# Kernel tuning notes

Hardware: AMD Instinct MI355X
Metric: run time of the kernel (lower is better)

Reference implementation:

```python
import math
import jax, jax.numpy as jnp
import numpy as np

DRAGON_ITERATIONS = 12
DRAGON_SMOOTHING = 0.1


def _dragon_patterns(iterations=DRAGON_ITERATIONS, smoothing=DRAGON_SMOOTHING):
    """Deterministic (non-learned) Dragon curve patterns, matching torch impl."""
    patterns = [np.array([0.5], dtype=np.float32)]
    kernel = np.ones(3, dtype=np.float32) / 3.0
    for _ in range(1, iterations):
        prev = patterns[-1]
        n = len(prev)
        newp = np.zeros(2 * n + 1, dtype=np.float32)
        newp[:n] = prev
        newp[n] = 0.5
        newp[n + 1:] = 1.0 - prev[::-1]
        if smoothing > 0:
            # conv1d with kernel_size=3, padding=1 (zero pad) == np.convolve 'same'
            newp = np.convolve(newp, kernel, mode='same').astype(np.float32)
        newp = (newp - newp.min()) / (newp.max() - newp.min() + 1e-8)
        patterns.append(newp.astype(np.float32))
    return patterns

_PATTERNS = _dragon_patterns()


def _interp_pattern(seq_len):
    """Linearly interpolate selected dragon pattern to seq_len (static shapes)."""
    it = min(int(math.log2(seq_len)), DRAGON_ITERATIONS - 1)
    pattern = _PATTERNS[it]
    if len(pattern) == seq_len:
        w = pattern.copy()
    else:
        x_old = np.linspace(0.0, 1.0, len(pattern), dtype=np.float64)
        x_new = np.linspace(0.0, 1.0, seq_len, dtype=np.float64)
        w = np.interp(x_new, x_old, pattern.astype(np.float64)).astype(np.float32)
    return it, jnp.asarray(w)


def setup_inputs() -> dict:
    key = jax.random.key(0)
    ks = jax.random.split(key, 8)
    B, S, D = 8, 2048, 512
    query = jax.random.normal(ks[0], (B, S, D), dtype=jnp.float32)
    k = jax.random.normal(ks[1], (B, S, D), dtype=jnp.float32)
    value = jax.random.normal(ks[2], (B, S, D), dtype=jnp.float32)
    pattern_scale = jnp.ones((DRAGON_ITERATIONS,), dtype=jnp.float32)
    pattern_bias = jnp.zeros((DRAGON_ITERATIONS,), dtype=jnp.float32)
    w1 = jax.random.normal(ks[3], (DRAGON_ITERATIONS, 64), dtype=jnp.float32) * (1.0 / math.sqrt(DRAGON_ITERATIONS))
    b1 = jnp.zeros((64,), dtype=jnp.float32)
    w2 = jax.random.normal(ks[4], (64, 1), dtype=jnp.float32) * (1.0 / 8.0)
    b2 = jnp.zeros((1,), dtype=jnp.float32)
    return {"query": query, "key": k, "value": value,
            "pattern_scale": pattern_scale, "pattern_bias": pattern_bias,
            "w1": w1, "b1": b1, "w2": w2, "b2": b2}


def reference(query, key, value, pattern_scale, pattern_bias, w1, b1, w2, b2):
    B, S, D = key.shape
    it, base_w = _interp_pattern(S)
    # learned affine + softplus on dragon weights
    dragon_w = jax.nn.softplus(base_w * pattern_scale[it] + pattern_bias[it])  # [S]
    weighted_keys = key * dragon_w[None, :, None]                              # [B,S,D]
    scores = jnp.einsum('bqd,bkd->bqk', query, weighted_keys) / math.sqrt(D)   # [B,S,S]
    attn = jax.nn.softmax(scores, axis=-1)
    # blend factor from one-hot iteration features through tiny MLP
    feat = jax.nn.one_hot(it, DRAGON_ITERATIONS, dtype=query.dtype)            # [12]
    h = jax.nn.relu(feat @ w1 + b1)
    blend = jax.nn.sigmoid(h @ w2 + b2)                                        # [1]
    blend = blend[0]
    final_attn = blend * attn + (1.0 - blend) / S                              # uniform blend
    out = jnp.einsum('bqk,bkd->bqd', final_attn, value)                        # [B,S,D]
    # original does output.squeeze(1); S>1 so it's a no-op here
    return out
```

## Files before the change

### kernel.cpp

```cpp
#include <hip/hip_runtime.h>
#include <cstdint>

#define DEV __device__ __forceinline__

typedef float f32x4 __attribute__((ext_vector_type(4)));
typedef short s16x8 __attribute__((ext_vector_type(8)));

DEV unsigned short f2bf(float f){
    unsigned u = __builtin_bit_cast(unsigned, f);
    u = u + 0x7fffu + ((u >> 16) & 1u);
    return (unsigned short)(u >> 16);
}
DEV float bf2f(unsigned short h){
    unsigned u = ((unsigned)h) << 16;
    return __builtin_bit_cast(float, u);
}

typedef const void __attribute__((address_space(1)))* gcp;
typedef void __attribute__((address_space(3)))* lp;
DEV void gload_lds16(const void* g, void* l){
    __builtin_amdgcn_global_load_lds((gcp)g, (lp)l, 16, 0, 0);
}

#define SCALE_QK 0.04419417382415922f

__global__ __launch_bounds__(256) void k_conv(
    const float* __restrict__ Q, const float* __restrict__ K,
    const float* __restrict__ V,
    const float* __restrict__ scale, const float* __restrict__ bias,
    const float* __restrict__ w1, const float* __restrict__ b1,
    const float* __restrict__ w2, const float* __restrict__ b2,
    unsigned short* __restrict__ Qb, unsigned short* __restrict__ Kb,
    unsigned short* __restrict__ Vt, float* __restrict__ vmean,
    float* __restrict__ dragon_wq, float* __restrict__ blend_out)
{
    __shared__ float sh[8200];
    int tid = threadIdx.x;
    int bx  = blockIdx.x;

    if (bx < 1024){
        const long long total4 = (long long)8*2048*512/4;
        long long stride = 1024LL*256;
        for (long long i = (long long)bx*256 + tid; i < total4; i += stride){
            long long base = i*4;
            const float4 q = *(const float4*)(Q + base);
            const float4 k = *(const float4*)(K + base);
            ushort4 qo, ko;
            qo.x = f2bf(q.x); qo.y = f2bf(q.y); qo.z = f2bf(q.z); qo.w = f2bf(q.w);
            ko.x = f2bf(k.x); ko.y = f2bf(k.y); ko.z = f2bf(k.z); ko.w = f2bf(k.w);
            *(ushort4*)(Qb + base) = qo;
            *(ushort4*)(Kb + base) = ko;
        }
        return;
    }

    if (bx < 3072){
        int t = bx - 1024;
        int stile = t & 31, dtile = (t >> 5) & 7, b = t >> 8;
        int s0 = stile*64, d0 = dtile*64;
        float (*tile)[66] = (float(*)[66])sh;
        float* red = sh + 4224;
        int tx = tid & 63, ty = tid >> 6;
        const float* src = V + ((long long)b*2048 + s0)*512 + d0;
        #pragma unroll
        for (int r = 0; r < 16; ++r){
            int row = r*4 + ty;
            tile[row][tx] = src[(long long)row*512 + tx];
        }
        __syncthreads();
        unsigned short* dst = Vt + ((long long)b*512 + d0)*2048 + s0;
        #pragma unroll
        for (int r = 0; r < 16; ++r){
            int drow = r*4 + ty;
            dst[(long long)drow*2048 + tx] = f2bf(tile[tx][drow]);
        }
        int dcol = tid & 63, sp = tid >> 6;
        float s = 0.f;
        #pragma unroll
        for (int ii = 0; ii < 16; ++ii) s += tile[sp*16 + ii][dcol];
        red[sp*64 + dcol] = s;
        __syncthreads();
        if (sp == 0){
            float tot = red[dcol] + red[64+dcol] + red[128+dcol] + red[192+dcol];
            atomicAdd(&vmean[b*512 + d0 + dcol], tot * (1.0f/2048.0f));
        }
        return;
    }

    float* A    = sh;
    float* Bb   = sh + 4095;
    float* red8 = sh + 8190;
    int lane = tid & 63, w = tid >> 6;
    if (tid == 0) A[0] = 0.5f;
    __syncthreads();
    float lo = 0.f, rden = 1.f;
    int len = 1;
    const float third = 1.0f/3.0f;
    for (int it = 1; it < 12; ++it){
        int n = len, nl = 2*n + 1;
        for (int i = tid; i < nl; i += 256){
            float v;
            if (i < n)       v = (A[i] - lo) * rden;
            else if (i == n) v = 0.5f;
            else             v = 1.0f - (A[2*n - i] - lo) * rden;
            Bb[i] = v;
        }
        __syncthreads();
        float mn = 3.4e38f, mx = -3.4e38f;
        for (int i = tid; i < nl; i += 256){
            float s = Bb[i];
            if (i > 0)    s += Bb[i-1];
            if (i < nl-1) s += Bb[i+1];
            s *= third;
            A[i] = s;
            mn = fminf(mn, s); mx = fmaxf(mx, s);
        }
        #pragma unroll
        for (int off = 32; off > 0; off >>= 1){
            mn = fminf(mn, __shfl_xor(mn, off, 64));
            mx = fmaxf(mx, __shfl_xor(mx, off, 64));
        }
        if (lane == 0){ red8[w] = mn; red8[4 + w] = mx; }
        __syncthreads();
        mn = fminf(fminf(red8[0], red8[1]), fminf(red8[2], red8[3]));
        mx = fmaxf(fmaxf(red8[4], red8[5]), fmaxf(red8[6], red8[7]));
        lo = mn; rden = 1.0f / (mx - mn + 1e-8f);
        len = nl;
        __syncthreads();
    }
    float sc = scale[11], bi = bias[11];
    for (int i = tid; i < 2048; i += 256){
        float x = (A[2*i] - lo) * rden * sc + bi;
        dragon_wq[i] = (fmaxf(x, 0.f) + log1pf(__expf(-fabsf(x)))) * SCALE_QK;
    }
    if (tid < 64){
        float h = fmaxf(w1[11*64 + tid] + b1[tid], 0.f);
        float c = h * w2[tid];
        for (int off = 32; off > 0; off >>= 1) c += __shfl_xor(c, off, 64);
        if (tid == 0) blend_out[0] = 1.f/(1.f + __expf(-(c + b2[0])));
    }
}

__global__ __launch_bounds__(256) void k_gemm_qk(
    const unsigned short* __restrict__ Qb, const unsigned short* __restrict__ Kb,
    const float* __restrict__ dragon_wq, unsigned short* __restrict__ Sp)
{
    __shared__ unsigned short At[128*64];
    __shared__ unsigned short Bt[128*64];
    int tid = threadIdx.x;
    int lane = tid & 63, wave = tid >> 6;
    int wm = wave >> 1, wn = wave & 1;
    int ln = lane & 15, q4 = lane >> 4;
    int sx = ln & 7;
    int q0 = blockIdx.y*128, k0 = blockIdx.x*128, b = blockIdx.z;
    const unsigned short* Abase = Qb + ((long long)b*2048 + q0)*512;
    const unsigned short* Bbase = Kb + ((long long)b*2048 + k0)*512;

    f32x4 acc[4][4];
    #pragma unroll
    for (int i = 0; i < 4; ++i)
        #pragma unroll
        for (int j = 0; j < 4; ++j) acc[i][j] = (f32x4)0.0f;

    int cc = lane & 7, rg = lane >> 3;
    for (int kt = 0; kt < 8; ++kt){
        #pragma unroll
        for (int c = 0; c < 4; ++c){
            int chunk = wave*4 + c;
            int row = chunk*8 + rg;
            int gc  = cc ^ (row & 7);
            gload_lds16(Abase + (long long)row*512 + kt*64 + gc*8, &At[chunk*512]);
            gload_lds16(Bbase + (long long)row*512 + kt*64 + gc*8, &Bt[chunk*512]);
        }
        __syncthreads();
        #pragma unroll
        for (int ks = 0; ks < 2; ++ks){
            int cs = ((ks*4 + q4) ^ sx) * 8;
            s16x8 af[4], bfr[4];
            #pragma unroll
            for (int i = 0; i < 4; ++i)
                af[i] = *(const s16x8*)&At[(wm*64 + i*16 + ln)*64 + cs];
            #pragma unroll
            for (int j = 0; j < 4; ++j)
                bfr[j] = *(const s16x8*)&Bt[(wn*64 + j*16 + ln)*64 + cs];
            #pragma unroll
            for (int i = 0; i < 4; ++i)
                #pragma unroll
                for (int j = 0; j < 4; ++j)
                    acc[i][j] = __builtin_amdgcn_mfma_f32_16x16x32_bf16(af[i], bfr[j], acc[i][j], 0, 0, 0);
        }
        __syncthreads();
    }
    float wq[4];
    #pragma unroll
    for (int j = 0; j < 4; ++j) wq[j] = dragon_wq[k0 + wn*64 + j*16 + ln];
    unsigned short* outp = Sp + (long long)b*2048*2048;
    #pragma unroll
    for (int i = 0; i < 4; ++i){
        #pragma unroll
        for (int j = 0; j < 4; ++j){
            #pragma unroll
            for (int r = 0; r < 4; ++r){
                int q = q0 + wm*64 + i*16 + q4*4 + r;
                int k = k0 + wn*64 + j*16 + ln;
                outp[(long long)q*2048 + k] = f2bf(__expf(acc[i][j][r] * wq[j]));
            }
        }
    }
}

__global__ __launch_bounds__(256) void k_gemm_pv(
    const unsigned short* __restrict__ Sp, const unsigned short* __restrict__ Vt,
    const float* __restrict__ vmean, const float* __restrict__ blendp,
    float* __restrict__ out)
{
    __shared__ unsigned short At[128*64];
    __shared__ unsigned short Bt[128*64];
    __shared__ float l_sh[128];
    int tid = threadIdx.x;
    int lane = tid & 63, wave = tid >> 6;
    int wm = wave >> 1, wn = wave & 1;
    int ln = lane & 15, q4 = lane >> 4;
    int sx = ln & 7;

    int g    = blockIdx.x;
    int xcd  = g & 7, slot = g >> 3;
    int pair = xcd*16 + (slot >> 2);
    int dt   = slot & 3;
    int qt   = pair & 15, b = pair >> 4;
    int q0 = qt*128, d0 = dt*128;

    const unsigned short* Abase = Sp + (long long)b*2048*2048 + (long long)q0*2048;
    const unsigned short* Bbase = Vt + ((long long)b*512 + d0)*2048;

    f32x4 acc[4][4];
    #pragma unroll
    for (int i = 0; i < 4; ++i)
        #pragma unroll
        for (int j = 0; j < 4; ++j) acc[i][j] = (f32x4)0.0f;
    float lsum[4] = {0.f, 0.f, 0.f, 0.f};

    int cc = lane & 7, rg = lane >> 3;
    for (int kt = 0; kt < 32; ++kt){
        #pragma unroll
        for (int c = 0; c < 4; ++c){
            int chunk = wave*4 + c;
            int row = chunk*8 + rg;
            int gc  = cc ^ (row & 7);
            gload_lds16(Abase + (long long)row*2048 + kt*64 + gc*8, &At[chunk*512]);
            gload_lds16(Bbase + (long long)row*2048 + kt*64 + gc*8, &Bt[chunk*512]);
        }
        __syncthreads();
        #pragma unroll
        for (int ks = 0; ks < 2; ++ks){
            int cs = ((ks*4 + q4) ^ sx) * 8;
            s16x8 af[4], bfr[4];
            #pragma unroll
            for (int i = 0; i < 4; ++i)
                af[i] = *(const s16x8*)&At[(wm*64 + i*16 + ln)*64 + cs];
            #pragma unroll
            for (int j = 0; j < 4; ++j)
                bfr[j] = *(const s16x8*)&Bt[(wn*64 + j*16 + ln)*64 + cs];
            if (wn == 0){
                #pragma unroll
                for (int i = 0; i < 4; ++i){
                    float s = 0.f;
                    #pragma unroll
                    for (int jj = 0; jj < 8; ++jj) s += bf2f((unsigned short)af[i][jj]);
                    lsum[i] += s;
                }
            }
            #pragma unroll
            for (int i = 0; i < 4; ++i)
                #pragma unroll
                for (int j = 0; j < 4; ++j)
                    acc[i][j] = __builtin_amdgcn_mfma_f32_16x16x32_bf16(af[i], bfr[j], acc[i][j], 0, 0, 0);
        }
        __syncthreads();
    }
    if (wn == 0){
        #pragma unroll
        for (int i = 0; i < 4; ++i){
            float v = lsum[i];
            v += __shfl_xor(v, 16, 64);
            v += __shfl_xor(v, 32, 64);
            if (lane < 16) l_sh[wm*64 + i*16 + lane] = v;
        }
    }
    __syncthreads();

    float blend = blendp[0];
    float ib = 1.0f - blend;
    float* obase = out + ((long long)b*2048 + q0)*512 + d0;
    float vm[4];
    #pragma unroll
    for (int j = 0; j < 4; ++j) vm[j] = vmean[b*512 + d0 + wn*64 + j*16 + ln];
    #pragma unroll
    for (int i = 0; i < 4; ++i){
        #pragma unroll
        for (int r = 0; r < 4; ++r){
            int ql = wm*64 + i*16 + q4*4 + r;
            float linv = 1.0f / l_sh[ql];
            #pragma unroll
            for (int j = 0; j < 4; ++j){
                int dl = wn*64 + j*16 + ln;
                obase[(long long)ql*512 + dl] = blend*acc[i][j][r]*linv + ib*vm[j];
            }
        }
    }
}

extern "C" void kernel_launch(void* const* d_in, const int* in_sizes, int n_in,
                              void* d_out, int out_size, void* d_ws, size_t ws_size,
                              hipStream_t stream)
{
    (void)in_sizes; (void)n_in; (void)out_size; (void)ws_size;
    const float* Q  = (const float*)d_in[0];
    const float* K  = (const float*)d_in[1];
    const float* V  = (const float*)d_in[2];
    const float* ps = (const float*)d_in[3];
    const float* pb = (const float*)d_in[4];
    const float* w1 = (const float*)d_in[5];
    const float* b1 = (const float*)d_in[6];
    const float* w2 = (const float*)d_in[7];
    const float* b2 = (const float*)d_in[8];
    float* out = (float*)d_out;

    char* ws = (char*)d_ws;
    float* dragon_wq       = (float*)(ws);
    float* blend           = (float*)(ws + 8192);
    float* vmean           = (float*)(ws + 16384);
    size_t off = 32768;
    unsigned short* Qb     = (unsigned short*)(ws + off);
    unsigned short* Kb     = (unsigned short*)(ws + off + (size_t)16*1024*1024);
    unsigned short* Vt     = (unsigned short*)(ws + off + (size_t)32*1024*1024);
    unsigned short* Sp     = (unsigned short*)(ws + off + (size_t)48*1024*1024);

    hipMemsetAsync(vmean, 0, 4096*sizeof(float), stream);
    hipLaunchKernelGGL(k_conv,    dim3(3073),      dim3(256), 0, stream,
                       Q, K, V, ps, pb, w1, b1, w2, b2, Qb, Kb, Vt, vmean, dragon_wq, blend);
    hipLaunchKernelGGL(k_gemm_qk, dim3(16, 16, 8), dim3(256), 0, stream,
                       Qb, Kb, dragon_wq, Sp);
    hipLaunchKernelGGL(k_gemm_pv, dim3(512),       dim3(256), 0, stream,
                       Sp, Vt, vmean, blend, out);
}
```

Measured before the change: 264.0 us.

## Precompute dragon pattern at compile time and stage QK epilogue through LDS

The serial single-block dragon-pattern construction (a long tail block in k_conv) is replaced by a constexpr table in device memory. The softplus weights are computed in the QK GEMM epilogue, and the blend MLP is computed per block in the PV kernel. The QK epilogue now writes bf16 scores into padded shared memory and stores them to global memory as coalesced 16-byte rows, instead of scattered 2-byte stores. This adds an extra LDS round trip and barrier, and the compile-time table may differ slightly from the runtime computation in floating-point rounding.

```diff
diff --git a/kernel.cpp b/kernel.cpp
--- a/kernel.cpp
+++ b/kernel.cpp
@@ -24,17 +24,41 @@
 
 #define SCALE_QK 0.04419417382415922f
 
+struct Pat2 { float v[2048]; };
+constexpr Pat2 make_pat2(){
+    float a[4095] = {}; float b[4095] = {};
+    a[0] = 0.5f; int len = 1;
+    for (int it = 1; it < 12; ++it){
+        int n = len, nl = 2*n + 1;
+        for (int i = 0; i < nl; ++i)
+            b[i] = (i < n) ? a[i] : ((i == n) ? 0.5f : 1.0f - a[2*n - i]);
+        const float third = 1.0f/3.0f;
+        float mn = 3.4e38f, mx = -3.4e38f;
+        for (int i = 0; i < nl; ++i){
+            float s = b[i]*third;
+            if (i > 0)      s += b[i-1]*third;
+            if (i < nl - 1) s += b[i+1]*third;
+            a[i] = s;
+            mn = (s < mn) ? s : mn;
+            mx = (s > mx) ? s : mx;
+        }
+        float d = mx - mn + 1e-8f;
+        for (int i = 0; i < nl; ++i) a[i] = (a[i] - mn) / d;
+        len = nl;
+    }
+    Pat2 p{};
+    for (int i = 0; i < 2048; ++i) p.v[i] = a[2*i];
+    return p;
+}
+__device__ const Pat2 g_pat2 = make_pat2();
+
 __global__ __launch_bounds__(256) void k_conv(
     const float* __restrict__ Q, const float* __restrict__ K,
     const float* __restrict__ V,
-    const float* __restrict__ scale, const float* __restrict__ bias,
-    const float* __restrict__ w1, const float* __restrict__ b1,
-    const float* __restrict__ w2, const float* __restrict__ b2,
     unsigned short* __restrict__ Qb, unsigned short* __restrict__ Kb,
-    unsigned short* __restrict__ Vt, float* __restrict__ vmean,
-    float* __restrict__ dragon_wq, float* __restrict__ blend_out)
+    unsigned short* __restrict__ Vt, float* __restrict__ vmean)
 {
-    __shared__ float sh[8200];
+    __shared__ float sh[4480];
     int tid = threadIdx.x;
     int bx  = blockIdx.x;
 
@@ -54,99 +78,47 @@
         return;
     }
 
-    if (bx < 3072){
-        int t = bx - 1024;
-        int stile = t & 31, dtile = (t >> 5) & 7, b = t >> 8;
-        int s0 = stile*64, d0 = dtile*64;
-        float (*tile)[66] = (float(*)[66])sh;
-        float* red = sh + 4224;
-        int tx = tid & 63, ty = tid >> 6;
-        const float* src = V + ((long long)b*2048 + s0)*512 + d0;
-        #pragma unroll
-        for (int r = 0; r < 16; ++r){
-            int row = r*4 + ty;
-            tile[row][tx] = src[(long long)row*512 + tx];
-        }
-        __syncthreads();
-        unsigned short* dst = Vt + ((long long)b*512 + d0)*2048 + s0;
-        #pragma unroll
-        for (int r = 0; r < 16; ++r){
-            int drow = r*4 + ty;
-            dst[(long long)drow*2048 + tx] = f2bf(tile[tx][drow]);
-        }
-        int dcol = tid & 63, sp = tid >> 6;
-        float s = 0.f;
-        #pragma unroll
-        for (int ii = 0; ii < 16; ++ii) s += tile[sp*16 + ii][dcol];
-        red[sp*64 + dcol] = s;
-        __syncthreads();
-        if (sp == 0){
-            float tot = red[dcol] + red[64+dcol] + red[128+dcol] + red[192+dcol];
-            atomicAdd(&vmean[b*512 + d0 + dcol], tot * (1.0f/2048.0f));
-        }
-        return;
-    }
-
-    float* A    = sh;
-    float* Bb   = sh + 4095;
-    float* red8 = sh + 8190;
-    int lane = tid & 63, w = tid >> 6;
-    if (tid == 0) A[0] = 0.5f;
+    int t = bx - 1024;
+    int stile = t & 31, dtile = (t >> 5) & 7, b = t >> 8;
+    int s0 = stile*64, d0 = dtile*64;
+    float (*tile)[66] = (float(*)[66])sh;
+    float* red = sh + 4224;
+    int tx = tid & 63, ty = tid >> 6;
+    const float* src = V + ((long long)b*2048 + s0)*512 + d0;
+    #pragma unroll
+    for (int r = 0; r < 16; ++r){
+        int row = r*4 + ty;
+        tile[row][tx] = src[(long long)row*512 + tx];
+    }
     __syncthreads();
-    float lo = 0.f, rden = 1.f;
-    int len = 1;
-    const float third = 1.0f/3.0f;
-    for (int it = 1; it < 12; ++it){
-        int n = len, nl = 2*n + 1;
-        for (int i = tid; i < nl; i += 256){
-            float v;
-            if (i < n)       v = (A[i] - lo) * rden;
-            else if (i == n) v = 0.5f;
-            else             v = 1.0f - (A[2*n - i] - lo) * rden;
-            Bb[i] = v;
-        }
-        __syncthreads();
-        float mn = 3.4e38f, mx = -3.4e38f;
-        for (int i = tid; i < nl; i += 256){
-            float s = Bb[i];
-            if (i > 0)    s += Bb[i-1];
-            if (i < nl-1) s += Bb[i+1];
-            s *= third;
-            A[i] = s;
-            mn = fminf(mn, s); mx = fmaxf(mx, s);
-        }
-        #pragma unroll
-        for (int off = 32; off > 0; off >>= 1){
-            mn = fminf(mn, __shfl_xor(mn, off, 64));
-            mx = fmaxf(mx, __shfl_xor(mx, off, 64));
-        }
-        if (lane == 0){ red8[w] = mn; red8[4 + w] = mx; }
-        __syncthreads();
-        mn = fminf(fminf(red8[0], red8[1]), fminf(red8[2], red8[3]));
-        mx = fmaxf(fmaxf(red8[4], red8[5]), fmaxf(red8[6], red8[7]));
-        lo = mn; rden = 1.0f / (mx - mn + 1e-8f);
-        len = nl;
-        __syncthreads();
-    }
-    float sc = scale[11], bi = bias[11];
-    for (int i = tid; i < 2048; i += 256){
-        float x = (A[2*i] - lo) * rden * sc + bi;
-        dragon_wq[i] = (fmaxf(x, 0.f) + log1pf(__expf(-fabsf(x)))) * SCALE_QK;
-    }
-    if (tid < 64){
-        float h = fmaxf(w1[11*64 + tid] + b1[tid], 0.f);
-        float c = h * w2[tid];
-        for (int off = 32; off > 0; off >>= 1) c += __shfl_xor(c, off, 64);
-        if (tid == 0) blend_out[0] = 1.f/(1.f + __expf(-(c + b2[0])));
-    }
-}
+    unsigned short* dst = Vt + ((long long)b*512 + d0)*2048 + s0;
+    #pragma unroll
+    for (int r = 0; r < 16; ++r){
+        int drow = r*4 + ty;
+        dst[(long long)drow*2048 + tx] = f2bf(tile[tx][drow]);
+    }
+    int dcol = tid & 63, sp = tid >> 6;
+    float s = 0.f;
+    #pragma unroll
+    for (int ii = 0; ii < 16; ++ii) s += tile[sp*16 + ii][dcol];
+    red[sp*64 + dcol] = s;
+    __syncthreads();
+    if (sp == 0){
+        float tot = red[dcol] + red[64+dcol] + red[128+dcol] + red[192+dcol];
+        atomicAdd(&vmean[b*512 + d0 + dcol], tot * (1.0f/2048.0f));
+    }
+}
+
+#define EPAD 140
 
 __global__ __launch_bounds__(256) void k_gemm_qk(
     const unsigned short* __restrict__ Qb, const unsigned short* __restrict__ Kb,
-    const float* __restrict__ dragon_wq, unsigned short* __restrict__ Sp)
+    const float* __restrict__ scale, const float* __restrict__ bias,
+    unsigned short* __restrict__ Sp)
 {
-    __shared__ unsigned short At[128*64];
-    __shared__ unsigned short Bt[128*64];
+    __shared__ unsigned short smem[128*EPAD];
+    unsigned short* At = smem;
+    unsigned short* Bt = smem + 8192;
     int tid = threadIdx.x;
     int lane = tid & 63, wave = tid >> 6;
     int wm = wave >> 1, wn = wave & 1;
@@ -191,37 +163,58 @@
         }
         __syncthreads();
     }
+
+    float sc = scale[11], bi = bias[11];
     float wq[4];
     #pragma unroll
-    for (int j = 0; j < 4; ++j) wq[j] = dragon_wq[k0 + wn*64 + j*16 + ln];
-    unsigned short* outp = Sp + (long long)b*2048*2048;
-    #pragma unroll
-    for (int i = 0; i < 4; ++i){
-        #pragma unroll
-        for (int j = 0; j < 4; ++j){
+    for (int j = 0; j < 4; ++j){
+        float x = g_pat2.v[k0 + wn*64 + j*16 + ln]*sc + bi;
+        wq[j] = (fmaxf(x, 0.f) + log1pf(__expf(-fabsf(x)))) * SCALE_QK;
+    }
+    #pragma unroll
+    for (int i = 0; i < 4; ++i)
+        #pragma unroll
+        for (int j = 0; j < 4; ++j)
             #pragma unroll
             for (int r = 0; r < 4; ++r){
-                int q = q0 + wm*64 + i*16 + q4*4 + r;
-                int k = k0 + wn*64 + j*16 + ln;
-                outp[(long long)q*2048 + k] = f2bf(__expf(acc[i][j][r] * wq[j]));
+                int ql = wm*64 + i*16 + q4*4 + r;
+                int kl = wn*64 + j*16 + ln;
+                smem[ql*EPAD + kl] = f2bf(__expf(acc[i][j][r] * wq[j]));
             }
-        }
-    }
+    __syncthreads();
+    int row = tid >> 1, half = tid & 1;
+    unsigned short* dstp = Sp + (long long)b*2048*2048
+                              + (long long)(q0 + row)*2048 + k0 + half*64;
+    const unsigned short* srcp = &smem[row*EPAD + half*64];
+    #pragma unroll
+    for (int u = 0; u < 8; ++u)
+        *(s16x8*)(dstp + u*8) = *(const s16x8*)(srcp + u*8);
 }
 
 __global__ __launch_bounds__(256) void k_gemm_pv(
     const unsigned short* __restrict__ Sp, const unsigned short* __restrict__ Vt,
-    const float* __restrict__ vmean, const float* __restrict__ blendp,
+    const float* __restrict__ vmean,
+    const float* __restrict__ w1, const float* __restrict__ b1,
+    const float* __restrict__ w2, const float* __restrict__ b2,
     float* __restrict__ out)
 {
     __shared__ unsigned short At[128*64];
     __shared__ unsigned short Bt[128*64];
     __shared__ float l_sh[128];
+    __shared__ float sh_blend;
     int tid = threadIdx.x;
     int lane = tid & 63, wave = tid >> 6;
     int wm = wave >> 1, wn = wave & 1;
     int ln = lane & 15, q4 = lane >> 4;
     int sx = ln & 7;
+
+    if (wave == 0){
+        float h = fmaxf(w1[11*64 + lane] + b1[lane], 0.f);
+        float c = h * w2[lane];
+        #pragma unroll
+        for (int off = 32; off > 0; off >>= 1) c += __shfl_xor(c, off, 64);
+        if (lane == 0) sh_blend = 1.f/(1.f + __expf(-(c + b2[0])));
+    }
 
     int g    = blockIdx.x;
     int xcd  = g & 7, slot = g >> 3;
@@ -289,7 +282,7 @@
     }
     __syncthreads();
 
-    float blend = blendp[0];
+    float blend = sh_blend;
     float ib = 1.0f - blend;
     float* obase = out + ((long long)b*2048 + q0)*512 + d0;
     float vm[4];
@@ -327,9 +320,7 @@
     float* out = (float*)d_out;
 
     char* ws = (char*)d_ws;
-    float* dragon_wq       = (float*)(ws);
-    float* blend           = (float*)(ws + 8192);
-    float* vmean           = (float*)(ws + 16384);
+    float* vmean           = (float*)(ws);
     size_t off = 32768;
     unsigned short* Qb     = (unsigned short*)(ws + off);
     unsigned short* Kb     = (unsigned short*)(ws + off + (size_t)16*1024*1024);
@@ -337,10 +328,10 @@
     unsigned short* Sp     = (unsigned short*)(ws + off + (size_t)48*1024*1024);
 
     hipMemsetAsync(vmean, 0, 4096*sizeof(float), stream);
-    hipLaunchKernelGGL(k_conv,    dim3(3073),      dim3(256), 0, stream,
-                       Q, K, V, ps, pb, w1, b1, w2, b2, Qb, Kb, Vt, vmean, dragon_wq, blend);
+    hipLaunchKernelGGL(k_conv,    dim3(3072),      dim3(256), 0, stream,
+                       Q, K, V, Qb, Kb, Vt, vmean);
     hipLaunchKernelGGL(k_gemm_qk, dim3(16, 16, 8), dim3(256), 0, stream,
-                       Qb, Kb, dragon_wq, Sp);
+                       Qb, Kb, ps, pb, Sp);
     hipLaunchKernelGGL(k_gemm_pv, dim3(512),       dim3(256), 0, stream,
-                       Sp, Vt, vmean, blend, out);
-}
+                       Sp, Vt, vmean, w1, b1, w2, b2, out);
+}
```

After: 266.2 us. No clear change (+0.9%).
